# Kernel tuning notes

Hardware: AMD Instinct MI355X
Metric: run time of the kernel (lower is better)

The kernel has to match this reference:

```python
import jax, jax.numpy as jnp
import numpy as np

N_CELLS_RNA, N_GENES = 8000, 8000
N_CELLS_ATAC, N_REGIONS = 8000, 20000
N_FACTORS = 100

def setup_inputs() -> dict:
    key = jax.random.key(0)
    ks = jax.random.split(key, 10)
    return {
        "G": jax.random.uniform(ks[0], (N_CELLS_RNA, N_GENES), jnp.float32),
        "R": jax.random.uniform(ks[1], (N_CELLS_ATAC, N_REGIONS), jnp.float32),
        "A": jax.random.uniform(ks[2], (N_GENES, N_REGIONS), jnp.float32),
        "C_1": jax.random.uniform(ks[3], (N_CELLS_RNA, N_FACTORS), jnp.float32),
        "C_2": jax.random.uniform(ks[4], (N_CELLS_ATAC, N_FACTORS), jnp.float32),
        "C_g": jax.random.uniform(ks[5], (N_GENES, N_FACTORS), jnp.float32),
        "C_r": jax.random.uniform(ks[6], (N_REGIONS, N_FACTORS), jnp.float32),
        "A_g": jax.random.normal(ks[7], (N_FACTORS, N_FACTORS), jnp.float32),
        "A_r": jax.random.normal(ks[8], (N_FACTORS, N_FACTORS), jnp.float32),
        "b_g": jnp.zeros((1, N_GENES), jnp.float32),
        "b_r": jnp.zeros((1, N_REGIONS), jnp.float32),
        "b_1": jnp.zeros((N_CELLS_RNA, 1), jnp.float32),
        "b_2": jnp.zeros((N_CELLS_ATAC, 1), jnp.float32),
        "alpha": jnp.array([1000.0, 1000.0, 100.0, 10.0, 0.0], jnp.float32),
    }

def reference(G, R, A, C_1, C_2, C_g, C_r, A_g, A_r, b_g, b_r, b_1, b_2, alpha):
    sm = lambda X: jax.nn.softmax(X, axis=1)  # row-wise softmax as in torch dim=1
    S1, S2, Sg, Sr = sm(C_1), sm(C_2), sm(C_g), sm(C_r)
    # loss1: RNA reconstruction. [n1,N]@[N,N] then @[N,ng]
    rec_G = (S1 @ A_g) @ Sg.T
    loss1 = jnp.mean(jnp.square(G - rec_G - b_g - b_1))
    # loss2: ATAC reconstruction
    rec_R = (S2 @ A_r) @ Sr.T
    loss2 = jnp.mean(jnp.square(R - rec_R - b_r - b_2))
    # loss3: -trace(A_r^T A_g) / ||A_r|| / ||A_g||
    loss3 = -jnp.sum(A_r * A_g) / jnp.linalg.norm(A_r) / jnp.linalg.norm(A_g)
    # loss4: -trace(Sg^T (A Sr)) / ||Sg|| / ||A Sr||  (trace via elementwise sum)
    ASr = A @ Sr  # [ng, N]
    loss4 = -jnp.sum(Sg * ASr) / jnp.linalg.norm(Sg) / jnp.linalg.norm(ASr)
    l1 = alpha[0] * loss1
    l2 = alpha[1] * loss2
    l3 = alpha[2] * loss3
    l4 = alpha[3] * loss4
    loss = l1 + l2 + l3 + l4
    return jnp.stack([loss, l1, l2, l3, l4])
```

## Files before the change

### kernel.cpp

```cpp
#include <hip/hip_runtime.h>
#include <hip/hip_bf16.h>

typedef __bf16 bf16x8 __attribute__((ext_vector_type(8)));
typedef float  f32x4  __attribute__((ext_vector_type(4)));
typedef unsigned short us4 __attribute__((ext_vector_type(4)));
typedef unsigned short us8 __attribute__((ext_vector_type(8)));

#define N_CELLS 8000
#define N_GENES 8000
#define N_REG   20000
#define NF      100
#define KP      128
#define NFT     112
#define KSPLIT  25
#define NWIN    625

static __device__ __forceinline__ unsigned short f2bf_bits(float f) {
  unsigned u = __builtin_bit_cast(unsigned, f);
  u = (u + 0x7FFFu + ((u >> 16) & 1u)) >> 16;
  return (unsigned short)u;
}
static __device__ __forceinline__ float bf2f(unsigned short s) {
  unsigned u = ((unsigned)s) << 16;
  return __builtin_bit_cast(float, u);
}
static __device__ __forceinline__ bf16x8 cvt8n(f32x4 v0, f32x4 v1) {
  bf16x8 r;
  r[0] = __builtin_bit_cast(__bf16, __float2bfloat16(v0[0]));
  r[1] = __builtin_bit_cast(__bf16, __float2bfloat16(v0[1]));
  r[2] = __builtin_bit_cast(__bf16, __float2bfloat16(v0[2]));
  r[3] = __builtin_bit_cast(__bf16, __float2bfloat16(v0[3]));
  r[4] = __builtin_bit_cast(__bf16, __float2bfloat16(v1[0]));
  r[5] = __builtin_bit_cast(__bf16, __float2bfloat16(v1[1]));
  r[6] = __builtin_bit_cast(__bf16, __float2bfloat16(v1[2]));
  r[7] = __builtin_bit_cast(__bf16, __float2bfloat16(v1[3]));
  return r;
}

__global__ __launch_bounds__(256) void pre_kernel(
    const float* __restrict__ C1, const float* __restrict__ C2,
    const float* __restrict__ Cg, const float* __restrict__ Cr,
    const float* __restrict__ Ag, const float* __restrict__ Ar,
    unsigned short* __restrict__ T1, unsigned short* __restrict__ T2,
    unsigned short* __restrict__ Sg, unsigned short* __restrict__ Sr,
    float* __restrict__ accv) {
  __shared__ float srow[4][NF];
  int b = blockIdx.x, t = threadIdx.x;
  int w = t >> 6, lane = t & 63;
  if (b == 11000) {
    float d = 0.f, na = 0.f, nr = 0.f;
    for (int i = t; i < NF * NF; i += 256) {
      float a = Ag[i], r = Ar[i];
      d = fmaf(a, r, d); na = fmaf(a, a, na); nr = fmaf(r, r, nr);
    }
    #pragma unroll
    for (int off = 32; off > 0; off >>= 1) {
      d += __shfl_xor(d, off); na += __shfl_xor(na, off); nr += __shfl_xor(nr, off);
    }
    __shared__ float r3[3][4];
    if (lane == 0) { r3[0][w] = d; r3[1][w] = na; r3[2][w] = nr; }
    __syncthreads();
    if (t == 0) {
      accv[2] = r3[0][0] + r3[0][1] + r3[0][2] + r3[0][3];
      accv[3] = r3[1][0] + r3[1][1] + r3[1][2] + r3[1][3];
      accv[4] = r3[2][0] + r3[2][1] + r3[2][2] + r3[2][3];
    }
    return;
  }
  const float* C; const float* W = nullptr;
  unsigned short* outR = nullptr; unsigned short* outT = nullptr;
  int i;
  if (b < 2000)      { C = C1; W = Ag; outT = T1; i = b * 4 + w; }
  else if (b < 4000) { C = C2; W = Ar; outT = T2; i = (b - 2000) * 4 + w; }
  else if (b < 6000) { C = Cg; outR = Sg; i = (b - 4000) * 4 + w; }
  else               { C = Cr; outR = Sr; i = (b - 6000) * 4 + w; }

  float v0 = C[i * NF + lane];
  float v1 = (lane < 36) ? C[i * NF + 64 + lane] : -3.0e38f;
  float m = fmaxf(v0, v1);
  #pragma unroll
  for (int off = 32; off > 0; off >>= 1) m = fmaxf(m, __shfl_xor(m, off));
  float e0 = __expf(v0 - m);
  float e1 = (lane < 36) ? __expf(v1 - m) : 0.f;
  float s = e0 + e1;
  #pragma unroll
  for (int off = 32; off > 0; off >>= 1) s += __shfl_xor(s, off);
  float inv = 1.f / s;
  e0 *= inv; e1 *= inv;

  if (outT == nullptr) {
    outR[i * KP + lane] = f2bf_bits(e0);
    outR[i * KP + 64 + lane] = (lane < 36) ? f2bf_bits(e1) : (unsigned short)0;
    return;
  }
  srow[w][lane] = e0;
  if (lane < 36) srow[w][64 + lane] = e1;
  __syncthreads();
  int c2 = 64 + lane;
  int c2c = (c2 < NF) ? c2 : NF - 1;
  float a0=0.f, a1=0.f, a2=0.f, a3=0.f;
  float d0=0.f, d1=0.f, d2=0.f, d3=0.f;
  #pragma unroll 4
  for (int k = 0; k < NF; k += 4) {
    float s0 = srow[w][k], s1 = srow[w][k+1], s2 = srow[w][k+2], s3 = srow[w][k+3];
    a0 = fmaf(s0, W[(k  )*NF + lane], a0);
    a1 = fmaf(s1, W[(k+1)*NF + lane], a1);
    a2 = fmaf(s2, W[(k+2)*NF + lane], a2);
    a3 = fmaf(s3, W[(k+3)*NF + lane], a3);
    d0 = fmaf(s0, W[(k  )*NF + c2c], d0);
    d1 = fmaf(s1, W[(k+1)*NF + c2c], d1);
    d2 = fmaf(s2, W[(k+2)*NF + c2c], d2);
    d3 = fmaf(s3, W[(k+3)*NF + c2c], d3);
  }
  outT[i * KP + lane] = f2bf_bits((a0 + a1) + (a2 + a3));
  outT[i * KP + c2]   = (c2 < NF) ? f2bf_bits((d0 + d1) + (d2 + d3)) : (unsigned short)0;
}

__global__ __launch_bounds__(256) void bpack_kernel(
    const unsigned short* __restrict__ Sr,
    unsigned short* __restrict__ Bpack) {
  __shared__ unsigned short lds[64 * 128];
  int t = threadIdx.x;
  long r0 = (long)blockIdx.x * 64;
  int w0 = blockIdx.x * 2;
  int nv = (int)((N_REG - r0 < 64) ? (N_REG - r0) : 64);
  #pragma unroll
  for (int q = 0; q < 4; ++q) {
    int idx = q * 256 + t;
    int row = idx >> 4, col8 = (idx & 15) * 8;
    us8 v = {0, 0, 0, 0, 0, 0, 0, 0};
    if (row < nv) v = *reinterpret_cast<const us8*>(Sr + (r0 + row) * KP + col8);
    *reinterpret_cast<us8*>(lds + row * 128 + col8) = v;
  }
  __syncthreads();
  for (int idx = t; idx < 896; idx += 256) {
    int win = idx >> 9;
    int rem = idx - win * 448;
    win = idx / 448; rem = idx - win * 448;
    int ni = rem >> 6, lane = rem & 63;
    int lr = lane & 15, lg = lane >> 4;
    if (w0 + win < NWIN) {
      us8 v;
      #pragma unroll
      for (int e = 0; e < 8; ++e)
        v[e] = lds[(win * 32 + lg * 8 + e) * 128 + ni * 16 + lr];
      *reinterpret_cast<us8*>(Bpack + (((long)(w0 + win) * 7 + ni) << 9) + (lane << 3)) = v;
    }
  }
}

__global__ __launch_bounds__(256, 3) void resid_kernel(
    const float* __restrict__ X,
    const unsigned short* __restrict__ Tm,
    const unsigned short* __restrict__ Sm,
    const float* __restrict__ bcol,
    const float* __restrict__ brow,
    int N, float* __restrict__ buckets) {
  __shared__ char ldsbuf[49152];
  char* ldsT = ldsbuf;
  char* ldsS = ldsbuf + 16384;
  int t = threadIdx.x;
  int wid = t >> 6, lane = t & 63;
  int lr = lane & 15, lg = lane >> 4;
  long r0blk = (long)blockIdx.y * 64;
  long c0blk = (long)blockIdx.x * 128;
  int r0 = (wid >> 1) * 32;
  int c0 = (wid & 1) * 64;

  bf16x8 sT[4], sS[8];
  #pragma unroll
  for (int i2 = 0; i2 < 4; ++i2) {
    int g = i2 * 256 + t, row = g >> 4, gi = g & 15;
    sT[i2] = *reinterpret_cast<const bf16x8*>(Tm + (r0blk + row) * KP + gi * 8);
  }
  #pragma unroll
  for (int i2 = 0; i2 < 8; ++i2) {
    int g = i2 * 256 + t, row = g >> 4, gi = g & 15;
    sS[i2] = *reinterpret_cast<const bf16x8*>(Sm + (c0blk + row) * KP + gi * 8);
  }

  f32x4 xv[2][4];
  #pragma unroll
  for (int ri = 0; ri < 2; ++ri) {
    long row = r0blk + r0 + ri * 16 + lr;
    #pragma unroll
    for (int ci = 0; ci < 4; ++ci) {
      long cb = c0blk + c0 + ci * 16 + lg * 4;
      if (cb < N) xv[ri][ci] = __builtin_nontemporal_load(
                    reinterpret_cast<const f32x4*>(X + row * N + cb));
      else        xv[ri][ci] = f32x4{0.f, 0.f, 0.f, 0.f};
    }
  }

  #pragma unroll
  for (int i2 = 0; i2 < 4; ++i2) {
    int g = i2 * 256 + t, row = g >> 4, gi = g & 15;
    int off = row * 256 + ((gi * 16) ^ ((row & 7) << 4));
    *reinterpret_cast<bf16x8*>(ldsT + off) = sT[i2];
  }
  #pragma unroll
  for (int i2 = 0; i2 < 8; ++i2) {
    int g = i2 * 256 + t, row = g >> 4, gi = g & 15;
    int off = row * 256 + ((gi * 16) ^ ((row & 7) << 4));
    *reinterpret_cast<bf16x8*>(ldsS + off) = sS[i2];
  }
  __syncthreads();

  f32x4 zero = {0.f, 0.f, 0.f, 0.f};
  f32x4 acc[4][2] = {{zero, zero}, {zero, zero}, {zero, zero}, {zero, zero}};
  #pragma unroll
  for (int ks = 0; ks < 4; ++ks) {
    bf16x8 a[4], bfr[2];
    #pragma unroll
    for (int ci = 0; ci < 4; ++ci) {
      int row = c0 + ci * 16 + lr;
      int off = row * 256 + (((ks * 64) + (lg * 16)) ^ ((row & 7) << 4));
      a[ci] = *reinterpret_cast<const bf16x8*>(ldsS + off);
    }
    #pragma unroll
    for (int ri = 0; ri < 2; ++ri) {
      int row = r0 + ri * 16 + lr;
      int off = row * 256 + (((ks * 64) + (lg * 16)) ^ ((row & 7) << 4));
      bfr[ri] = *reinterpret_cast<const bf16x8*>(ldsT + off);
    }
    #pragma unroll
    for (int ci = 0; ci < 4; ++ci)
      #pragma unroll
      for (int ri = 0; ri < 2; ++ri)
        acc[ci][ri] = __builtin_amdgcn_mfma_f32_16x16x32_bf16(a[ci], bfr[ri], acc[ci][ri], 0, 0, 0);
  }

  float brv[2];
  #pragma unroll
  for (int ri = 0; ri < 2; ++ri) brv[ri] = brow[r0blk + r0 + ri * 16 + lr];

  float sse = 0.f;
  #pragma unroll
  for (int ci = 0; ci < 4; ++ci) {
    long cb = c0blk + c0 + ci * 16 + lg * 4;
    if (cb < N) {
      f32x4 bc = *reinterpret_cast<const f32x4*>(bcol + cb);
      #pragma unroll
      for (int ri = 0; ri < 2; ++ri) {
        f32x4 x = xv[ri][ci];
        #pragma unroll
        for (int j = 0; j < 4; ++j) {
          float e = x[j] - acc[ci][ri][j] - bc[j] - brv[ri];
          sse = fmaf(e, e, sse);
        }
      }
    }
  }
  #pragma unroll
  for (int off = 32; off > 0; off >>= 1) sse += __shfl_xor(sse, off);
  __shared__ float wsum[4];
  if (lane == 0) wsum[wid] = sse;
  __syncthreads();
  if (t == 0)
    atomicAdd(&buckets[(blockIdx.y * gridDim.x + blockIdx.x) & 63],
              wsum[0] + wsum[1] + wsum[2] + wsum[3]);
}

__global__ __launch_bounds__(256, 4) void asr_kernel(
    const float* __restrict__ A,
    const unsigned short* __restrict__ Bpack,
    float* __restrict__ ASrN) {
  __shared__ char lds[2][16384];
  int t = threadIdx.x;
  int w = t >> 6, lane = t & 63;
  int lr = lane & 15, lg = lane >> 4;
  int gBase = blockIdx.x * 64;
  int kb0 = blockIdx.y * 800;
  int wk0 = blockIdx.y * 25;

  f32x4 zero = {0.f, 0.f, 0.f, 0.f};
  f32x4 acc[7] = {zero, zero, zero, zero, zero, zero, zero};
  f32x4 sreg[8];

  #pragma unroll
  for (int p = 0; p < 4; ++p) {
    int flat = p * 2048 + t * 8;
    int row = flat >> 7, kk = flat & 127;
    const float* src = A + (long)(gBase + row) * N_REG + kb0 + kk;
    sreg[2 * p]     = __builtin_nontemporal_load(reinterpret_cast<const f32x4*>(src));
    sreg[2 * p + 1] = __builtin_nontemporal_load(reinterpret_cast<const f32x4*>(src + 4));
  }

  #pragma unroll 1
  for (int it = 0; it < 7; ++it) {
    char* buf = lds[it & 1];
    if (it < 6) {
      #pragma unroll
      for (int p = 0; p < 4; ++p) {
        int flat = p * 2048 + t * 8;
        int row = flat >> 7, kk = flat & 127;
        int off = row * 256 + ((kk * 2) ^ ((row & 7) << 4));
        *reinterpret_cast<bf16x8*>(buf + off) = cvt8n(sreg[2 * p], sreg[2 * p + 1]);
      }
    } else {
      int row = t >> 2, kk = (t & 3) * 8;
      int off = row * 256 + ((kk * 2) ^ ((row & 7) << 4));
      *reinterpret_cast<bf16x8*>(buf + off) = cvt8n(sreg[0], sreg[1]);
    }
    __syncthreads();

    if (it < 5) {
      #pragma unroll
      for (int p = 0; p < 4; ++p) {
        int flat = p * 2048 + t * 8;
        int row = flat >> 7, kk = flat & 127;
        const float* src = A + (long)(gBase + row) * N_REG + kb0 + (it + 1) * 128 + kk;
        sreg[2 * p]     = __builtin_nontemporal_load(reinterpret_cast<const f32x4*>(src));
        sreg[2 * p + 1] = __builtin_nontemporal_load(reinterpret_cast<const f32x4*>(src + 4));
      }
    } else if (it == 5) {
      int row = t >> 2, kk = (t & 3) * 8;
      const float* src = A + (long)(gBase + row) * N_REG + kb0 + 768 + kk;
      sreg[0] = __builtin_nontemporal_load(reinterpret_cast<const f32x4*>(src));
      sreg[1] = __builtin_nontemporal_load(reinterpret_cast<const f32x4*>(src + 4));
    }

    int arow = w * 16 + lr;
    int nk = (it < 6) ? 4 : 1;
    #pragma unroll 4
    for (int ks = 0; ks < nk; ++ks) {
      int off = arow * 256 + (((ks * 64) + lg * 16) ^ ((arow & 7) << 4));
      bf16x8 ag = *reinterpret_cast<const bf16x8*>(buf + off);
      long wbase = ((long)(wk0 + it * 4 + ks) * 7) << 9;
      #pragma unroll
      for (int ni = 0; ni < 7; ++ni) {
        bf16x8 b = *reinterpret_cast<const bf16x8*>(
            Bpack + wbase + ((long)ni << 9) + (lane << 3));
        acc[ni] = __builtin_amdgcn_mfma_f32_16x16x32_bf16(ag, b, acc[ni], 0, 0, 0);
      }
    }
  }

  float* slice = ASrN + (long)blockIdx.y * (N_GENES * NFT);
  int g0 = gBase + w * 16;
  #pragma unroll
  for (int ni = 0; ni < 7; ++ni) {
    int f = ni * 16 + lr;
    #pragma unroll
    for (int j = 0; j < 4; ++j)
      __builtin_nontemporal_store(acc[ni][j], &slice[(g0 + lg * 4 + j) * NFT + f]);
  }
}

__global__ void l4red_kernel(const unsigned short* __restrict__ Sgbf,
                             const float* __restrict__ ASrN,
                             float* __restrict__ accv) {
  const int NV = N_GENES * NFT / 4;
  int t = blockIdx.x * blockDim.x + threadIdx.x;
  float d = 0.f, n1 = 0.f, n2 = 0.f;
  for (int q = t; q < NV; q += gridDim.x * blockDim.x) {
    int g = q / (NFT / 4);
    int f4 = (q - g * (NFT / 4)) * 4;
    f32x4 av = {0.f, 0.f, 0.f, 0.f};
    #pragma unroll
    for (int s = 0; s < KSPLIT; ++s)
      av += __builtin_nontemporal_load(
              reinterpret_cast<const f32x4*>(ASrN + (long)s * (N_GENES * NFT) + g * NFT + f4));
    us4 sgb = *reinterpret_cast<const us4*>(Sgbf + g * KP + f4);
    #pragma unroll
    for (int j = 0; j < 4; ++j) {
      float sg = bf2f(sgb[j]);
      d = fmaf(sg, av[j], d); n1 = fmaf(sg, sg, n1); n2 = fmaf(av[j], av[j], n2);
    }
  }
  #pragma unroll
  for (int off = 32; off > 0; off >>= 1) {
    d += __shfl_xor(d, off); n1 += __shfl_xor(n1, off); n2 += __shfl_xor(n2, off);
  }
  __shared__ float r3[3][4];
  int lane = threadIdx.x & 63, w = threadIdx.x >> 6;
  if (lane == 0) { r3[0][w] = d; r3[1][w] = n1; r3[2][w] = n2; }
  __syncthreads();
  if (threadIdx.x == 0) {
    atomicAdd(&accv[5], r3[0][0] + r3[0][1] + r3[0][2] + r3[0][3]);
    atomicAdd(&accv[6], r3[1][0] + r3[1][1] + r3[1][2] + r3[1][3]);
    atomicAdd(&accv[7], r3[2][0] + r3[2][1] + r3[2][2] + r3[2][3]);
  }
}

__global__ void fin_kernel(const float* __restrict__ accv,
                           const float* __restrict__ bk1,
                           const float* __restrict__ bk2,
                           const float* __restrict__ alpha,
                           float* __restrict__ out) {
  if (threadIdx.x == 0) {
    float s1 = 0.f, s2 = 0.f;
    for (int i = 0; i < 64; ++i) { s1 += bk1[i]; s2 += bk2[i]; }
    float loss1 = s1 / 64000000.0f;
    float loss2 = s2 / 160000000.0f;
    float loss3 = -accv[2] / (sqrtf(accv[3]) * sqrtf(accv[4]));
    float loss4 = -accv[5] / (sqrtf(accv[6]) * sqrtf(accv[7]));
    float l1 = alpha[0] * loss1, l2 = alpha[1] * loss2;
    float l3 = alpha[2] * loss3, l4 = alpha[3] * loss4;
    out[0] = l1 + l2 + l3 + l4;
    out[1] = l1; out[2] = l2; out[3] = l3; out[4] = l4;
  }
}


extern "C" void kernel_launch(void* const* d_in, const int* in_sizes, int n_in,
                              void* d_out, int out_size, void* d_ws, size_t ws_size,
                              hipStream_t stream) {
  const float* G  = (const float*)d_in[0];
  const float* R  = (const float*)d_in[1];
  const float* A  = (const float*)d_in[2];
  const float* C1 = (const float*)d_in[3];
  const float* C2 = (const float*)d_in[4];
  const float* Cg = (const float*)d_in[5];
  const float* Cr = (const float*)d_in[6];
  const float* Ag = (const float*)d_in[7];
  const float* Ar = (const float*)d_in[8];
  const float* bg = (const float*)d_in[9];
  const float* br = (const float*)d_in[10];
  const float* b1 = (const float*)d_in[11];
  const float* b2 = (const float*)d_in[12];
  const float* alpha = (const float*)d_in[13];

  char* ws = (char*)d_ws;
  float* accv           = (float*)(ws + 0);
  float* buckets1       = (float*)(ws + 64);
  float* buckets2       = (float*)(ws + 320);
  float* ASrN           = (float*)(ws + 1024);
  unsigned short* T1    = (unsigned short*)(ws + 89601024);
  unsigned short* T2    = (unsigned short*)(ws + 91649024);
  unsigned short* Sg    = (unsigned short*)(ws + 93697024);
  unsigned short* Sr    = (unsigned short*)(ws + 95745024);
  unsigned short* Bpack = (unsigned short*)(ws + 100865024);

  hipMemsetAsync(d_ws, 0, 576, stream);

  pre_kernel<<<11001, 256, 0, stream>>>(C1, C2, Cg, Cr, Ag, Ar,
                                        T1, T2, Sg, Sr, accv);
  bpack_kernel<<<313, 256, 0, stream>>>(Sr, Bpack);

  resid_kernel<<<dim3(63, 125), 256, 0, stream>>>(G, T1, Sg, bg, b1, N_GENES, buckets1);
  resid_kernel<<<dim3(157, 125), 256, 0, stream>>>(R, T2, Sr, br, b2, N_REG, buckets2);

  asr_kernel<<<dim3(125, KSPLIT), 256, 0, stream>>>(A, Bpack, ASrN);

  l4red_kernel<<<128, 256, 0, stream>>>(Sg, ASrN, accv);
  fin_kernel<<<1, 64, 0, stream>>>(accv, buckets1, buckets2, alpha, (float*)d_out);
}
```

Baseline: 566.3 us.

## Use single-wave asr blocks with two row tiles and swizzle ATAC resid grid

Measured after the change: 790.5 us. +39.6%, slower.

```diff
diff --git a/kernel.cpp b/kernel.cpp
--- a/kernel.cpp
+++ b/kernel.cpp
@@ -134,9 +134,7 @@
   }
   __syncthreads();
   for (int idx = t; idx < 896; idx += 256) {
-    int win = idx >> 9;
-    int rem = idx - win * 448;
-    win = idx / 448; rem = idx - win * 448;
+    int win = idx / 448, rem = idx - win * 448;
     int ni = rem >> 6, lane = rem & 63;
     int lr = lane & 15, lg = lane >> 4;
     if (w0 + win < NWIN) {
@@ -155,15 +153,21 @@
     const unsigned short* __restrict__ Sm,
     const float* __restrict__ bcol,
     const float* __restrict__ brow,
-    int N, float* __restrict__ buckets) {
+    int N, float* __restrict__ buckets, int swz) {
   __shared__ char ldsbuf[49152];
   char* ldsT = ldsbuf;
   char* ldsS = ldsbuf + 16384;
   int t = threadIdx.x;
   int wid = t >> 6, lane = t & 63;
   int lr = lane & 15, lg = lane >> 4;
-  long r0blk = (long)blockIdx.y * 64;
-  long c0blk = (long)blockIdx.x * 128;
+  int bx, by;
+  if (swz) {
+    int b = blockIdx.x;
+    if (b < 19500) { int sg = b / 500, rem = b - sg * 500; bx = sg * 4 + (rem & 3); by = rem >> 2; }
+    else           { bx = 156; by = b - 19500; }
+  } else { bx = blockIdx.x; by = blockIdx.y; }
+  long r0blk = (long)by * 64;
+  long c0blk = (long)bx * 128;
   int r0 = (wid >> 1) * 32;
   int c0 = (wid & 1) * 64;
 
@@ -261,89 +265,93 @@
               wsum[0] + wsum[1] + wsum[2] + wsum[3]);
 }
 
-__global__ __launch_bounds__(256, 4) void asr_kernel(
+__global__ __launch_bounds__(64, 4) void asr_kernel(
     const float* __restrict__ A,
     const unsigned short* __restrict__ Bpack,
     float* __restrict__ ASrN) {
-  __shared__ char lds[2][16384];
-  int t = threadIdx.x;
-  int w = t >> 6, lane = t & 63;
-  int lr = lane & 15, lg = lane >> 4;
-  int gBase = blockIdx.x * 64;
+  __shared__ char lds[2][4096];
+  int l = threadIdx.x;
+  int lr = l & 15, lg = l >> 4;
+  int g0 = blockIdx.x * 32;
   int kb0 = blockIdx.y * 800;
   int wk0 = blockIdx.y * 25;
 
+  int srow = l >> 1;
+  int sc0f = (l & 1) * 32;
+  const float* pa = A + (long)(g0 + srow) * N_REG + kb0 + sc0f;
+  const float* pa2 = A + (long)(g0 + srow) * N_REG + kb0 + 768 + (l & 1) * 16;
+
   f32x4 zero = {0.f, 0.f, 0.f, 0.f};
-  f32x4 acc[7] = {zero, zero, zero, zero, zero, zero, zero};
+  f32x4 acc[2][7];
+  #pragma unroll
+  for (int q = 0; q < 2; ++q)
+    #pragma unroll
+    for (int ni = 0; ni < 7; ++ni) acc[q][ni] = zero;
   f32x4 sreg[8];
 
   #pragma unroll
-  for (int p = 0; p < 4; ++p) {
-    int flat = p * 2048 + t * 8;
-    int row = flat >> 7, kk = flat & 127;
-    const float* src = A + (long)(gBase + row) * N_REG + kb0 + kk;
-    sreg[2 * p]     = __builtin_nontemporal_load(reinterpret_cast<const f32x4*>(src));
-    sreg[2 * p + 1] = __builtin_nontemporal_load(reinterpret_cast<const f32x4*>(src + 4));
-  }
+  for (int q = 0; q < 8; ++q)
+    sreg[q] = __builtin_nontemporal_load(reinterpret_cast<const f32x4*>(pa + q * 4));
 
   #pragma unroll 1
-  for (int it = 0; it < 7; ++it) {
+  for (int it = 0; it < 13; ++it) {
     char* buf = lds[it & 1];
-    if (it < 6) {
-      #pragma unroll
-      for (int p = 0; p < 4; ++p) {
-        int flat = p * 2048 + t * 8;
-        int row = flat >> 7, kk = flat & 127;
-        int off = row * 256 + ((kk * 2) ^ ((row & 7) << 4));
-        *reinterpret_cast<bf16x8*>(buf + off) = cvt8n(sreg[2 * p], sreg[2 * p + 1]);
+    if (it < 12) {
+      #pragma unroll
+      for (int q2 = 0; q2 < 4; ++q2) {
+        int colb = (l & 1) * 64 + q2 * 16;
+        int off = srow * 128 + (colb ^ ((srow & 7) << 4));
+        *reinterpret_cast<bf16x8*>(buf + off) = cvt8n(sreg[2 * q2], sreg[2 * q2 + 1]);
       }
     } else {
-      int row = t >> 2, kk = (t & 3) * 8;
-      int off = row * 256 + ((kk * 2) ^ ((row & 7) << 4));
-      *reinterpret_cast<bf16x8*>(buf + off) = cvt8n(sreg[0], sreg[1]);
-    }
-    __syncthreads();
-
-    if (it < 5) {
-      #pragma unroll
-      for (int p = 0; p < 4; ++p) {
-        int flat = p * 2048 + t * 8;
-        int row = flat >> 7, kk = flat & 127;
-        const float* src = A + (long)(gBase + row) * N_REG + kb0 + (it + 1) * 128 + kk;
-        sreg[2 * p]     = __builtin_nontemporal_load(reinterpret_cast<const f32x4*>(src));
-        sreg[2 * p + 1] = __builtin_nontemporal_load(reinterpret_cast<const f32x4*>(src + 4));
+      #pragma unroll
+      for (int q2 = 0; q2 < 2; ++q2) {
+        int colb = (l & 1) * 32 + q2 * 16;
+        int off = srow * 128 + (colb ^ ((srow & 7) << 4));
+        *reinterpret_cast<bf16x8*>(buf + off) = cvt8n(sreg[2 * q2], sreg[2 * q2 + 1]);
       }
-    } else if (it == 5) {
-      int row = t >> 2, kk = (t & 3) * 8;
-      const float* src = A + (long)(gBase + row) * N_REG + kb0 + 768 + kk;
-      sreg[0] = __builtin_nontemporal_load(reinterpret_cast<const f32x4*>(src));
-      sreg[1] = __builtin_nontemporal_load(reinterpret_cast<const f32x4*>(src + 4));
-    }
-
-    int arow = w * 16 + lr;
-    int nk = (it < 6) ? 4 : 1;
-    #pragma unroll 4
+    }
+    if (it < 11) {
+      #pragma unroll
+      for (int q = 0; q < 8; ++q)
+        sreg[q] = __builtin_nontemporal_load(
+            reinterpret_cast<const f32x4*>(pa + (it + 1) * 64 + q * 4));
+    } else if (it == 11) {
+      #pragma unroll
+      for (int q = 0; q < 4; ++q)
+        sreg[q] = __builtin_nontemporal_load(
+            reinterpret_cast<const f32x4*>(pa2 + q * 4));
+    }
+    int nk = (it < 12) ? 2 : 1;
+    #pragma unroll 2
     for (int ks = 0; ks < nk; ++ks) {
-      int off = arow * 256 + (((ks * 64) + lg * 16) ^ ((arow & 7) << 4));
-      bf16x8 ag = *reinterpret_cast<const bf16x8*>(buf + off);
-      long wbase = ((long)(wk0 + it * 4 + ks) * 7) << 9;
+      int cb = ks * 64 + lg * 16;
+      bf16x8 ar0 = *reinterpret_cast<const bf16x8*>(
+          buf + lr * 128 + (cb ^ ((lr & 7) << 4)));
+      bf16x8 ar1 = *reinterpret_cast<const bf16x8*>(
+          buf + (16 + lr) * 128 + (cb ^ (((16 + lr) & 7) << 4)));
+      long wbase = ((long)(wk0 + it * 2 + ks) * 7) << 9;
       #pragma unroll
       for (int ni = 0; ni < 7; ++ni) {
         bf16x8 b = *reinterpret_cast<const bf16x8*>(
-            Bpack + wbase + ((long)ni << 9) + (lane << 3));
-        acc[ni] = __builtin_amdgcn_mfma_f32_16x16x32_bf16(ag, b, acc[ni], 0, 0, 0);
+            Bpack + wbase + ((long)ni << 9) + (l << 3));
+        acc[0][ni] = __builtin_amdgcn_mfma_f32_16x16x32_bf16(ar0, b, acc[0][ni], 0, 0, 0);
+        acc[1][ni] = __builtin_amdgcn_mfma_f32_16x16x32_bf16(ar1, b, acc[1][ni], 0, 0, 0);
       }
     }
   }
 
   float* slice = ASrN + (long)blockIdx.y * (N_GENES * NFT);
-  int g0 = gBase + w * 16;
-  #pragma unroll
-  for (int ni = 0; ni < 7; ++ni) {
-    int f = ni * 16 + lr;
-    #pragma unroll
-    for (int j = 0; j < 4; ++j)
-      __builtin_nontemporal_store(acc[ni][j], &slice[(g0 + lg * 4 + j) * NFT + f]);
+  #pragma unroll
+  for (int q = 0; q < 2; ++q) {
+    int gb = g0 + q * 16 + lg * 4;
+    #pragma unroll
+    for (int ni = 0; ni < 7; ++ni) {
+      int f = ni * 16 + lr;
+      #pragma unroll
+      for (int j = 0; j < 4; ++j)
+        __builtin_nontemporal_store(acc[q][ni][j], &slice[(gb + j) * NFT + f]);
+    }
   }
 }
 
@@ -438,10 +446,12 @@
                                         T1, T2, Sg, Sr, accv);
   bpack_kernel<<<313, 256, 0, stream>>>(Sr, Bpack);
 
-  resid_kernel<<<dim3(63, 125), 256, 0, stream>>>(G, T1, Sg, bg, b1, N_GENES, buckets1);
-  resid_kernel<<<dim3(157, 125), 256, 0, stream>>>(R, T2, Sr, br, b2, N_REG, buckets2);
-
-  asr_kernel<<<dim3(125, KSPLIT), 256, 0, stream>>>(A, Bpack, ASrN);
+  resid_kernel<<<dim3(63, 125), 256, 0, stream>>>(G, T1, Sg, bg, b1, N_GENES,
+                                                  buckets1, 0);
+  resid_kernel<<<19625, 256, 0, stream>>>(R, T2, Sr, br, b2, N_REG,
+                                          buckets2, 1);
+
+  asr_kernel<<<dim3(250, KSPLIT), 64, 0, stream>>>(A, Bpack, ASrN);
 
   l4red_kernel<<<128, 256, 0, stream>>>(Sg, ASrN, accv);
   fin_kernel<<<1, 64, 0, stream>>>(accv, buckets1, buckets2, alpha, (float*)d_out);
```
